# Performance work log

Hardware: AMD Instinct MI355X
Metric: run time of the kernel (lower is better)

The kernel has to match this reference:

```python
import jax, jax.numpy as jnp
from jax import lax
import numpy as np

UNITS, S, B, T = 64, 16, 512, 4096
LOG_2PI = float(np.log(2.0 * np.pi))


def setup_inputs() -> dict:
    key = jax.random.key(0)
    k1, k2 = jax.random.split(key)
    inputs = jax.random.normal(k1, (B, T), dtype=jnp.float32)
    # positive 'probs' (TFP Categorical takes log internally)
    hmm_params = jax.random.uniform(k2, (UNITS, S, S), dtype=jnp.float32,
                                    minval=1e-3, maxval=1.0)
    return {"inputs": inputs, "hmm_params": hmm_params}


def reference(inputs, hmm_params):
    # --- HMM parameters, as TFP builds them ---
    trans = hmm_params[0]                      # (S, S) unnormalized probs
    log_A = jnp.log(trans) - jnp.log(trans.sum(-1, keepdims=True))  # (S,S) row-normalized
    init = hmm_params[0, 0]                    # (S,)
    log_pi = jnp.log(init) - jnp.log(init.sum())
    # Emission: Normal(loc=0, scale=1) per state -> same logp for every state
    emit = -0.5 * inputs * inputs - 0.5 * LOG_2PI   # [B, T]
    emit = emit[:, :, None]                          # [B, T, 1] broadcasts over S

    # --- Viterbi forward (max-product) ---
    delta0 = log_pi[None, :] + emit[:, 0]            # [B, S]
    emit_seq = jnp.moveaxis(emit[:, 1:], 1, 0)       # [T-1, B, 1]

    def step(delta, e_t):
        scores = delta[:, :, None] + log_A[None, :, :]   # [B, S_prev, S_cur]
        psi = jnp.argmax(scores, axis=1).astype(jnp.int32)  # [B, S]
        delta_new = jnp.max(scores, axis=1) + e_t            # [B, S]
        return delta_new, psi

    deltaT, psis = lax.scan(step, delta0, emit_seq)  # psis: [T-1, B, S]

    # --- Backtrace ---
    zT = jnp.argmax(deltaT, axis=-1).astype(jnp.int32)   # [B]

    def back(z, psi):
        z_prev = jnp.take_along_axis(psi, z[:, None], axis=1)[:, 0]
        return z_prev, z_prev

    _, zs = lax.scan(back, zT, psis, reverse=True)   # zs: [T-1, B] = states t=0..T-2
    path = jnp.concatenate([zs.T, zT[:, None]], axis=1)  # [B, T]
    return path
```

## Files before the change

### kernel.cpp

```cpp
#include <hip/hip_runtime.h>
#include <math.h>

#define T_LEN 4096
#define B_SZ  512
#define CH    128
#define NCH   32
#define PITCH 129
#define PHASES 34

typedef unsigned uv2 __attribute__((ext_vector_type(2)));

__device__ __forceinline__ float emis(float xv) {
    float a = __fmul_rn(-0.5f, xv);
    float b = __fmul_rn(a, xv);
    return __fsub_rn(b, (float)0.9189385332046727);
}

#define DPP_ROR0(K, SRC) __builtin_amdgcn_update_dpp(0, (SRC), 0x120 + (K), 0xF, 0xF, false)
#define M3(x, y, z) fmaxf(fmaxf(x, y), z)

#define ADP(DST, K)                                                                   \
    asm("v_add_f32_dpp %0, %1, %2 row_ror:" #K " row_mask:0xf bank_mask:0xf"          \
        : "=v"(DST) : "v"(dr), "v"(a[K]))

#define STEPC(ET)                                                                     \
    {                                                                                 \
        float s0 = __fadd_rn(dr, a[0]);                                               \
        float s1, s2, s3, s4, s5, s6, s7;                                             \
        ADP(s1, 1); ADP(s2, 2); ADP(s3, 3); ADP(s4, 4);                               \
        ADP(s5, 5); ADP(s6, 6); ADP(s7, 7);                                           \
        float u0 = M3(s0, s1, s2), u1 = M3(s3, s4, s5), u2 = fmaxf(s6, s7);           \
        float own = M3(u0, u1, u2);                                                   \
        unsigned ou = __float_as_uint(own);                                           \
        uv2 rr = __builtin_amdgcn_permlane32_swap(ou, ou, false, false);              \
        float m = M3(__uint_as_float(rr[0]), __uint_as_float(rr[1]), own);            \
        float t8 = __int_as_float(__builtin_amdgcn_update_dpp(                        \
            0, __float_as_int(m), 0x128, 0xF, 0xF, false));                           \
        dr = __fadd_rn(hi32 ? t8 : m, ET);                                            \
    }

#define GRP4(QV, SLOTDW)                                                              \
    {                                                                                 \
        float4 dq;                                                                    \
        STEPC(QV.x) dq.x = dr; STEPC(QV.y) dq.y = dr;                                 \
        STEPC(QV.z) dq.z = dr; STEPC(QV.w) dq.w = dr;                                 \
        if (lo32) *(float4*)(db + (SLOTDW)) = dq;                                     \
    }

#define PERMSEL(V, Q)                                                                 \
    {                                                                                 \
        int sel_ = (V) & 7;                                                           \
        int lo_, hi_;                                                                 \
        asm("v_perm_b32 %0, %1, %2, %3" : "=v"(lo_) : "v"((Q).y), "v"((Q).x), "v"(sel_)); \
        asm("v_perm_b32 %0, %1, %2, %3" : "=v"(hi_) : "v"((Q).w), "v"((Q).z), "v"(sel_)); \
        V = (((V) & 8) ? hi_ : lo_) & 0xff;                                           \
    }

#define WALKN(BASE, CUR, PRE, POST, START)                                            \
    {                                                                                 \
        uint4 m_[8];                                                                  \
        _Pragma("unroll") for (int z_ = 0; z_ < 8; ++z_)                              \
            m_[z_] = *(const uint4*)((BASE) + ((START) - z_) * 16);                   \
        for (int r_ = (START); r_ >= 15; r_ -= 8) {                                   \
            uint4 n_[8];                                                              \
            _Pragma("unroll") for (int z_ = 0; z_ < 8; ++z_)                          \
                n_[z_] = *(const uint4*)((BASE) + (r_ - 8 - z_) * 16);                \
            _Pragma("unroll") for (int z_ = 0; z_ < 8; ++z_) {                        \
                PRE(r_ - z_, CUR) PERMSEL(CUR, m_[z_]) POST(r_ - z_, CUR)             \
            }                                                                         \
            _Pragma("unroll") for (int z_ = 0; z_ < 8; ++z_) m_[z_] = n_[z_];         \
        }                                                                             \
        _Pragma("unroll") for (int z_ = 0; z_ < 8; ++z_) {                            \
            PRE(7 - z_, CUR) PERMSEL(CUR, m_[z_]) POST(7 - z_, CUR)                   \
        }                                                                             \
    }

#define NIBHOP(V, Q) (V) = (int)(((Q) >> ((unsigned)(V) << 2)) & 15ull);

#define NWALKN(BASE, CUR, POST, START)                                                \
    {                                                                                 \
        const unsigned long long* bb_ = (BASE);                                       \
        unsigned long long m_[8];                                                     \
        _Pragma("unroll") for (int z_ = 0; z_ < 8; ++z_) m_[z_] = bb_[(START) - z_];  \
        for (int r_ = (START); r_ >= 15; r_ -= 8) {                                   \
            unsigned long long n_[8];                                                 \
            _Pragma("unroll") for (int z_ = 0; z_ < 8; ++z_) n_[z_] = bb_[r_ - 8 - z_]; \
            _Pragma("unroll") for (int z_ = 0; z_ < 8; ++z_) {                        \
                NIBHOP(CUR, m_[z_]) POST(r_ - z_, CUR)                                \
            }                                                                         \
            _Pragma("unroll") for (int z_ = 0; z_ < 8; ++z_) m_[z_] = n_[z_];         \
        }                                                                             \
        _Pragma("unroll") for (int z_ = 0; z_ < 8; ++z_) {                            \
            NIBHOP(CUR, m_[z_]) POST(7 - z_, CUR)                                     \
        }                                                                             \
    }

#define NOPX(r, c)
#define EBL_PRE(r, c) eb[r] = (unsigned char)(c);
#define OUT_POST(r, c) ob[r] = (c);

#define RLF(V, L) __int_as_float(__builtin_amdgcn_readlane(__float_as_int(V), (L)))

#define PSI2_I(I, V, BL)                                                              \
    {                                                                                 \
        float cs_ = RLF(V, (BL) + (I));                                               \
        float sA_ = __fadd_rn(ddA[I], cs_);                                           \
        if (sA_ > bestA) argA = I;                           \
        bestA = fmaxf(bestA, sA_);                                                    \
        float sB_ = __fadd_rn(ddB[I], cs_);                                           \
        if (sB_ > bestB) argB = I;                                                    \
        bestB = fmaxf(bestB, sB_);                                                    \
    }

#define PSI2_J(JJ, V)                                                                 \
    {                                                                                 \
        float c0_ = RLF(V, (((JJ) & 3) * 16) + 0);                                    \
        float bestA = __fadd_rn(ddA[0], c0_); int argA = 0;                           \
        float bestB = __fadd_rn(ddB[0], c0_); int argB = 0;                           \
        PSI2_I(1, V, ((JJ) & 3) * 16)  PSI2_I(2, V, ((JJ) & 3) * 16)                  \
        PSI2_I(3, V, ((JJ) & 3) * 16)  PSI2_I(4, V, ((JJ) & 3) * 16)                  \
        PSI2_I(5, V, ((JJ) & 3) * 16)  PSI2_I(6, V, ((JJ) & 3) * 16)                  \
        PSI2_I(7, V, ((JJ) & 3) * 16)  PSI2_I(8, V, ((JJ) & 3) * 16)                  \
        PSI2_I(9, V, ((JJ) & 3) * 16)  PSI2_I(10, V, ((JJ) & 3) * 16)                 \
        PSI2_I(11, V, ((JJ) & 3) * 16) PSI2_I(12, V, ((JJ) & 3) * 16)                 \
        PSI2_I(13, V, ((JJ) & 3) * 16) PSI2_I(14, V, ((JJ) & 3) * 16)                 \
        PSI2_I(15, V, ((JJ) & 3) * 16)                                                \
        pkA |= (unsigned long long)argA << ((JJ) * 4);                                \
        pkB |= (unsigned long long)argB << ((JJ) * 4);                                \
    }

__global__ __launch_bounds__(256) void k_fused(const float* __restrict__ x,
                                               const float* __restrict__ hmm,
                                               int* __restrict__ out) {
    __shared__ __align__(16) float dbuf[2][2][16][132];
    __shared__ unsigned long long pnib[2][NCH * PITCH];
    __shared__ uint4 Mlv[2][NCH];
    __shared__ unsigned char Ebl[2][NCH];
    __shared__ float carry_l[2][16];
    __shared__ float logA_l[256];
    __shared__ float logAT_l[256];
    __shared__ __align__(16) float Ebuf[4][2][CH];

    const int tid = threadIdx.x;
    const int wave = tid >> 6;
    const int blk = blockIdx.x;

    {
        const int pi = tid >> 4, pj = tid & 15;
        const float* row = hmm + pi * 16;
        float r8[8];
#pragma unroll
        for (int k = 0; k < 8; ++k) r8[k] = __fadd_rn(row[k], row[k + 8]);
        float s = __fadd_rn(
            __fadd_rn(__fadd_rn(r8[0], r8[1]), __fadd_rn(r8[2], r8[3])),
            __fadd_rn(__fadd_rn(r8[4], r8[5]), __fadd_rn(r8[6], r8[7])));
        float la = (float)log((double)row[pj]);
        float ls = (float)log((double)s);
        float v = __fsub_rn(la, ls);
        logA_l[tid] = v;
        logAT_l[pj * 16 + pi] = v;
        const int cc0 = tid >> 7, gp = (tid >> 6) & 1, l0 = tid & 63;
        const size_t xb = (size_t)(blk * 2 + gp) * T_LEN + CH * cc0 + l0 + 1;
        Ebuf[cc0][gp][l0]      = emis(x[xb]);
        Ebuf[cc0][gp][l0 + 64] = emis(x[xb + 64]);
    }
    __syncthreads();

    if (wave == 0) {
        asm volatile("s_setprio 3");
        const int j = tid & 15;
        const int g = (tid >> 4) & 1;
        const int h = tid >> 5;
        const bool lo32 = (tid < 32);
        const bool hi32 = (tid >= 32);
        const int jh = (j + 8 * h) & 15;
        float a[8];
        float dr;
        float4 q0, q1, q2, q3;
        {
            a[0] = logA_l[jh * 16 + j];
#define LOADA(K) { int sk = DPP_ROR0(K, jh); a[K] = logA_l[sk * 16 + j]; }
            LOADA(1) LOADA(2) LOADA(3) LOADA(4) LOADA(5) LOADA(6) LOADA(7)
#undef LOADA
            const int b = blk * 2 + g;
            float e0 = emis(x[(size_t)b * T_LEN]);
            dr = __fadd_rn(logA_l[jh], e0);
            const float4* e0p = (const float4*)&Ebuf[0][g][0];
            q0 = e0p[0]; q1 = e0p[1]; q2 = e0p[2]; q3 = e0p[3];
        }
        for (int p = 0; p < PHASES; ++p) {
            __syncthreads();
            if (p < NCH) {
                float* db = &dbuf[p & 1][g][j][0];
                if (lo32) db[128] = dr;
                const float4* ecur = (const float4*)&Ebuf[p & 3][g][0];
                const float4* enxt = (const float4*)&Ebuf[(p + 1) & 3][g][0];
                if (p < NCH - 1) {
#pragma clang loop unroll(disable)
                    for (int ii = 0; ii < 7; ++ii) {
                        GRP4(q0, ii * 16 + 0)  q0 = ecur[(ii + 1) * 4 + 0];
                        GRP4(q1, ii * 16 + 4)  q1 = ecur[(ii + 1) * 4 + 1];
                        GRP4(q2, ii * 16 + 8)  q2 = ecur[(ii + 1) * 4 + 2];
                        GRP4(q3, ii * 16 + 12) q3 = ecur[(ii + 1) * 4 + 3];
                    }
                    GRP4(q0, 112) q0 = enxt[0];
                    GRP4(q1, 116) q1 = enxt[1];
                    GRP4(q2, 120) q2 = enxt[2];
                    GRP4(q3, 124) q3 = enxt[3];
                } else {
#pragma clang loop unroll(disable)
                    for (int ii = 0; ii < 7; ++ii) {
                        GRP4(q0, ii * 16 + 0)  q0 = ecur[(ii + 1) * 4 + 0];
                        GRP4(q1, ii * 16 + 4)  q1 = ecur[(ii + 1) * 4 + 1];
                        GRP4(q2, ii * 16 + 8)  q2 = ecur[(ii + 1) * 4 + 2];
                        GRP4(q3, ii * 16 + 12) q3 = ecur[(ii + 1) * 4 + 3];
                    }
                    GRP4(q0, 112) GRP4(q1, 116) GRP4(q2, 120)
                    STEPC(q3.x) if (lo32) db[124] = dr;
                    STEPC(q3.y) if (lo32) db[125] = dr;
                    STEPC(q3.z) if (lo32) db[126] = dr;
                }
            }
        }
        if (lo32) carry_l[g][j] = dr;
    } else if (wave <= 2) {
        const int g2 = wave - 1;
        const int r = tid & 63;
        float vq0 = logAT_l[r];
        float vq1 = logAT_l[64 + r];
        float vq2 = logAT_l[128 + r];
        float vq3 = logAT_l[192 + r];
        for (int p = 0; p < PHASES; ++p) {
            __syncthreads();
            const int c = p - 1;
            if (c >= 0 && c < NCH) {
                const int q = c & 1;
                const int rsA = (r == 0) ? 128 : (r - 1);
                const int rsB = r + 63;
                float ddA[16], ddB[16];
#pragma unroll
                for (int i = 0; i < 16; ++i) {
                    ddA[i] = dbuf[q][g2][i][rsA];
                    ddB[i] = dbuf[q][g2][i][rsB];
                }
                asm volatile("" : "+v"(vq0), "+v"(vq1), "+v"(vq2), "+v"(vq3));
                unsigned long long pkA = 0ull, pkB = 0ull;
                PSI2_J(0, vq0)  PSI2_J(1, vq0)  PSI2_J(2, vq0)  PSI2_J(3, vq0)
                PSI2_J(4, vq1)  PSI2_J(5, vq1)  PSI2_J(6, vq1)  PSI2_J(7, vq1)
                PSI2_J(8, vq2)  PSI2_J(9, vq2)  PSI2_J(10, vq2) PSI2_J(11, vq2)
                PSI2_J(12, vq3) PSI2_J(13, vq3) PSI2_J(14, vq3) PSI2_J(15, vq3)
                if (c == NCH - 1 && r == 63) pkB = 0xFEDCBA9876543210ull;
                pnib[g2][c * PITCH + r]      = pkA;
                pnib[g2][c * PITCH + r + 64] = pkB;
            }
        }
    } else {
        const int l = tid - 192;
        const int g3 = l >> 4, z = l & 15;
        for (int p = 0; p < PHASES; ++p) {
            __syncthreads();
            const int cc = p + 2;
            if (cc < NCH) {
                const int t1 = CH * cc + l + 1;
                const int t2 = t1 + 64;
                Ebuf[cc & 3][0][l] = emis(x[(size_t)(blk * 2 + 0) * T_LEN + t1]);
                Ebuf[cc & 3][1][l] = emis(x[(size_t)(blk * 2 + 1) * T_LEN + t1]);
                if (t2 <= T_LEN - 1) {
                    Ebuf[cc & 3][0][l + 64] = emis(x[(size_t)(blk * 2 + 0) * T_LEN + t2]);
                    Ebuf[cc & 3][1][l + 64] = emis(x[(size_t)(blk * 2 + 1) * T_LEN + t2]);
                }
            }
            const int c = p - 2;
            if (c >= 0 && l < 32) {
                int cur = z;
                NWALKN(&pnib[g3][c * PITCH], cur, NOPX, 127)
                ((unsigned char*)&Mlv[g3][c])[z] = (unsigned char)cur;
            }
        }
    }

    __syncthreads();
    if (tid < 2) {
        const int g = tid;
        float best = carry_l[g][0]; int zT = 0;
#pragma unroll
        for (int i = 1; i < 16; ++i) {
            float s = carry_l[g][i];
            if (s > best) zT = i;
            best = fmaxf(best, s);
        }
        int z = zT;
        unsigned char* eb = &Ebl[g][0];
        WALKN((const unsigned char*)&Mlv[g][0], z, EBL_PRE, NOPX, NCH - 1)
    }
    __syncthreads();
    if (tid < 64) {
        const int g = tid >> 5, c = tid & 31;
        int* ob = out + (size_t)(blk * 2 + g) * T_LEN + c * CH;
        int cur = Ebl[g][c];
        NWALKN(&pnib[g][c * PITCH], cur, OUT_POST, 127)
    }
}

extern "C" void kernel_launch(void* const* d_in, const int* in_sizes, int n_in,
                              void* d_out, int out_size, void* d_ws, size_t ws_size,
                              hipStream_t stream) {
    (void)in_sizes; (void)n_in; (void)out_size; (void)d_ws; (void)ws_size;
    const float* x   = (const float*)d_in[0];
    const float* hmm = (const float*)d_in[1];
    int* out = (int*)d_out;

    hipLaunchKernelGGL(k_fused, dim3(B_SZ / 2), dim3(256), 0, stream, x, hmm, out);
}
```

Baseline: 302.0 us.

## Process one batch row per block instead of two, doubling grid size

Each block now handles a single sequence rather than two, so the grid covers all 512 rows with 512 blocks. The forward wave uses only 16 lanes per step, the psi waves each take half of the 128 time positions for that one row, and all shared-memory buffers shrink by half. This cuts the serial work per block and spreads the rows over more blocks, trading for lower lane utilisation in the DPP recurrence wave and for doubling the per-block setup and sync overhead.

```diff
diff --git a/kernel.cpp b/kernel.cpp
--- a/kernel.cpp
+++ b/kernel.cpp
@@ -44,7 +44,7 @@
         float4 dq;                                                                    \
         STEPC(QV.x) dq.x = dr; STEPC(QV.y) dq.y = dr;                                 \
         STEPC(QV.z) dq.z = dr; STEPC(QV.w) dq.w = dr;                                 \
-        if (lo32) *(float4*)(db + (SLOTDW)) = dq;                                     \
+        if (lo16) *(float4*)(db + (SLOTDW)) = dq;                                     \
     }
 
 #define PERMSEL(V, Q)                                                                 \
@@ -101,49 +101,44 @@
 
 #define RLF(V, L) __int_as_float(__builtin_amdgcn_readlane(__float_as_int(V), (L)))
 
-#define PSI2_I(I, V, BL)                                                              \
-    {                                                                                 \
-        float cs_ = RLF(V, (BL) + (I));                                               \
-        float sA_ = __fadd_rn(ddA[I], cs_);                                           \
-        if (sA_ > bestA) argA = I;                           \
-        bestA = fmaxf(bestA, sA_);                                                    \
-        float sB_ = __fadd_rn(ddB[I], cs_);                                           \
-        if (sB_ > bestB) argB = I;                                                    \
-        bestB = fmaxf(bestB, sB_);                                                    \
-    }
-
-#define PSI2_J(JJ, V)                                                                 \
-    {                                                                                 \
-        float c0_ = RLF(V, (((JJ) & 3) * 16) + 0);                                    \
-        float bestA = __fadd_rn(ddA[0], c0_); int argA = 0;                           \
-        float bestB = __fadd_rn(ddB[0], c0_); int argB = 0;                           \
-        PSI2_I(1, V, ((JJ) & 3) * 16)  PSI2_I(2, V, ((JJ) & 3) * 16)                  \
-        PSI2_I(3, V, ((JJ) & 3) * 16)  PSI2_I(4, V, ((JJ) & 3) * 16)                  \
-        PSI2_I(5, V, ((JJ) & 3) * 16)  PSI2_I(6, V, ((JJ) & 3) * 16)                  \
-        PSI2_I(7, V, ((JJ) & 3) * 16)  PSI2_I(8, V, ((JJ) & 3) * 16)                  \
-        PSI2_I(9, V, ((JJ) & 3) * 16)  PSI2_I(10, V, ((JJ) & 3) * 16)                 \
-        PSI2_I(11, V, ((JJ) & 3) * 16) PSI2_I(12, V, ((JJ) & 3) * 16)                 \
-        PSI2_I(13, V, ((JJ) & 3) * 16) PSI2_I(14, V, ((JJ) & 3) * 16)                 \
-        PSI2_I(15, V, ((JJ) & 3) * 16)                                                \
-        pkA |= (unsigned long long)argA << ((JJ) * 4);                                \
-        pkB |= (unsigned long long)argB << ((JJ) * 4);                                \
+#define PSI1_I(I, V, BL)                                                              \
+    {                                                                                 \
+        float s_ = __fadd_rn(dd[I], RLF(V, (BL) + (I)));                              \
+        if (s_ > best) arg = I;                              \
+        best = fmaxf(best, s_);                                                       \
+    }
+
+#define PSI1_J(JJ, V)                                                                 \
+    {                                                                                 \
+        float best = __fadd_rn(dd[0], RLF(V, (((JJ) & 3) * 16) + 0));                 \
+        int arg = 0;                                                                  \
+        PSI1_I(1, V, ((JJ) & 3) * 16)  PSI1_I(2, V, ((JJ) & 3) * 16)                  \
+        PSI1_I(3, V, ((JJ) & 3) * 16)  PSI1_I(4, V, ((JJ) & 3) * 16)                  \
+        PSI1_I(5, V, ((JJ) & 3) * 16)  PSI1_I(6, V, ((JJ) & 3) * 16)                  \
+        PSI1_I(7, V, ((JJ) & 3) * 16)  PSI1_I(8, V, ((JJ) & 3) * 16)                  \
+        PSI1_I(9, V, ((JJ) & 3) * 16)  PSI1_I(10, V, ((JJ) & 3) * 16)                 \
+        PSI1_I(11, V, ((JJ) & 3) * 16) PSI1_I(12, V, ((JJ) & 3) * 16)                 \
+        PSI1_I(13, V, ((JJ) & 3) * 16) PSI1_I(14, V, ((JJ) & 3) * 16)                 \
+        PSI1_I(15, V, ((JJ) & 3) * 16)                                                \
+        pk |= (unsigned long long)arg << ((JJ) * 4);                                  \
     }
 
 __global__ __launch_bounds__(256) void k_fused(const float* __restrict__ x,
                                                const float* __restrict__ hmm,
                                                int* __restrict__ out) {
-    __shared__ __align__(16) float dbuf[2][2][16][132];
-    __shared__ unsigned long long pnib[2][NCH * PITCH];
-    __shared__ uint4 Mlv[2][NCH];
-    __shared__ unsigned char Ebl[2][NCH];
-    __shared__ float carry_l[2][16];
+    __shared__ __align__(16) float dbuf[2][16][132];
+    __shared__ unsigned long long pnib[NCH * PITCH];
+    __shared__ uint4 Mlv[NCH];
+    __shared__ unsigned char Ebl[NCH];
+    __shared__ float carry_l[16];
     __shared__ float logA_l[256];
     __shared__ float logAT_l[256];
-    __shared__ __align__(16) float Ebuf[4][2][CH];
+    __shared__ __align__(16) float Ebuf[4][CH];
 
     const int tid = threadIdx.x;
     const int wave = tid >> 6;
     const int blk = blockIdx.x;
+    const size_t xb = (size_t)blk * T_LEN;
 
     {
         const int pi = tid >> 4, pj = tid & 15;
@@ -159,19 +154,16 @@
         float v = __fsub_rn(la, ls);
         logA_l[tid] = v;
         logAT_l[pj * 16 + pi] = v;
-        const int cc0 = tid >> 7, gp = (tid >> 6) & 1, l0 = tid & 63;
-        const size_t xb = (size_t)(blk * 2 + gp) * T_LEN + CH * cc0 + l0 + 1;
-        Ebuf[cc0][gp][l0]      = emis(x[xb]);
-        Ebuf[cc0][gp][l0 + 64] = emis(x[xb + 64]);
+        const int cc0 = tid >> 7, pos = tid & 127;
+        Ebuf[cc0][pos] = emis(x[xb + CH * cc0 + pos + 1]);
     }
     __syncthreads();
 
     if (wave == 0) {
         asm volatile("s_setprio 3");
         const int j = tid & 15;
-        const int g = (tid >> 4) & 1;
         const int h = tid >> 5;
-        const bool lo32 = (tid < 32);
+        const bool lo16 = (tid < 16);
         const bool hi32 = (tid >= 32);
         const int jh = (j + 8 * h) & 15;
         float a[8];
@@ -182,19 +174,18 @@
 #define LOADA(K) { int sk = DPP_ROR0(K, jh); a[K] = logA_l[sk * 16 + j]; }
             LOADA(1) LOADA(2) LOADA(3) LOADA(4) LOADA(5) LOADA(6) LOADA(7)
 #undef LOADA
-            const int b = blk * 2 + g;
-            float e0 = emis(x[(size_t)b * T_LEN]);
+            float e0 = emis(x[xb]);
             dr = __fadd_rn(logA_l[jh], e0);
-            const float4* e0p = (const float4*)&Ebuf[0][g][0];
+            const float4* e0p = (const float4*)&Ebuf[0][0];
             q0 = e0p[0]; q1 = e0p[1]; q2 = e0p[2]; q3 = e0p[3];
         }
         for (int p = 0; p < PHASES; ++p) {
             __syncthreads();
             if (p < NCH) {
-                float* db = &dbuf[p & 1][g][j][0];
-                if (lo32) db[128] = dr;
-                const float4* ecur = (const float4*)&Ebuf[p & 3][g][0];
-                const float4* enxt = (const float4*)&Ebuf[(p + 1) & 3][g][0];
+                float* db = &dbuf[p & 1][j][0];
+                if (lo16) db[128] = dr;
+                const float4* ecur = (const float4*)&Ebuf[p & 3][0];
+                const float4* enxt = (const float4*)&Ebuf[(p + 1) & 3][0];
                 if (p < NCH - 1) {
 #pragma clang loop unroll(disable)
                     for (int ii = 0; ii < 7; ++ii) {
@@ -216,15 +207,15 @@
                         GRP4(q3, ii * 16 + 12) q3 = ecur[(ii + 1) * 4 + 3];
                     }
                     GRP4(q0, 112) GRP4(q1, 116) GRP4(q2, 120)
-                    STEPC(q3.x) if (lo32) db[124] = dr;
-                    STEPC(q3.y) if (lo32) db[125] = dr;
-                    STEPC(q3.z) if (lo32) db[126] = dr;
+                    STEPC(q3.x) if (lo16) db[124] = dr;
+                    STEPC(q3.y) if (lo16) db[125] = dr;
+                    STEPC(q3.z) if (lo16) db[126] = dr;
                 }
             }
         }
-        if (lo32) carry_l[g][j] = dr;
+        if (lo16) carry_l[j] = dr;
     } else if (wave <= 2) {
-        const int g2 = wave - 1;
+        const int half = wave - 1;
         const int r = tid & 63;
         float vq0 = logAT_l[r];
         float vq1 = logAT_l[64 + r];
@@ -235,70 +226,59 @@
             const int c = p - 1;
             if (c >= 0 && c < NCH) {
                 const int q = c & 1;
-                const int rsA = (r == 0) ? 128 : (r - 1);
-                const int rsB = r + 63;
-                float ddA[16], ddB[16];
+                const int rs = half ? (r + 63) : ((r == 0) ? 128 : (r - 1));
+                float dd[16];
 #pragma unroll
-                for (int i = 0; i < 16; ++i) {
-                    ddA[i] = dbuf[q][g2][i][rsA];
-                    ddB[i] = dbuf[q][g2][i][rsB];
-                }
+                for (int i = 0; i < 16; ++i) dd[i] = dbuf[q][i][rs];
                 asm volatile("" : "+v"(vq0), "+v"(vq1), "+v"(vq2), "+v"(vq3));
-                unsigned long long pkA = 0ull, pkB = 0ull;
-                PSI2_J(0, vq0)  PSI2_J(1, vq0)  PSI2_J(2, vq0)  PSI2_J(3, vq0)
-                PSI2_J(4, vq1)  PSI2_J(5, vq1)  PSI2_J(6, vq1)  PSI2_J(7, vq1)
-                PSI2_J(8, vq2)  PSI2_J(9, vq2)  PSI2_J(10, vq2) PSI2_J(11, vq2)
-                PSI2_J(12, vq3) PSI2_J(13, vq3) PSI2_J(14, vq3) PSI2_J(15, vq3)
-                if (c == NCH - 1 && r == 63) pkB = 0xFEDCBA9876543210ull;
-                pnib[g2][c * PITCH + r]      = pkA;
-                pnib[g2][c * PITCH + r + 64] = pkB;
+                unsigned long long pk = 0ull;
+                PSI1_J(0, vq0)  PSI1_J(1, vq0)  PSI1_J(2, vq0)  PSI1_J(3, vq0)
+                PSI1_J(4, vq1)  PSI1_J(5, vq1)  PSI1_J(6, vq1)  PSI1_J(7, vq1)
+                PSI1_J(8, vq2)  PSI1_J(9, vq2)  PSI1_J(10, vq2) PSI1_J(11, vq2)
+                PSI1_J(12, vq3) PSI1_J(13, vq3) PSI1_J(14, vq3) PSI1_J(15, vq3)
+                if (half && c == NCH - 1 && r == 63) pk = 0xFEDCBA9876543210ull;
+                pnib[c * PITCH + half * 64 + r] = pk;
             }
         }
     } else {
-        const int l = tid - 192;
-        const int g3 = l >> 4, z = l & 15;
+        const int l = tid & 63;
         for (int p = 0; p < PHASES; ++p) {
             __syncthreads();
             const int cc = p + 2;
             if (cc < NCH) {
                 const int t1 = CH * cc + l + 1;
                 const int t2 = t1 + 64;
-                Ebuf[cc & 3][0][l] = emis(x[(size_t)(blk * 2 + 0) * T_LEN + t1]);
-                Ebuf[cc & 3][1][l] = emis(x[(size_t)(blk * 2 + 1) * T_LEN + t1]);
-                if (t2 <= T_LEN - 1) {
-                    Ebuf[cc & 3][0][l + 64] = emis(x[(size_t)(blk * 2 + 0) * T_LEN + t2]);
-                    Ebuf[cc & 3][1][l + 64] = emis(x[(size_t)(blk * 2 + 1) * T_LEN + t2]);
-                }
+                Ebuf[cc & 3][l] = emis(x[xb + t1]);
+                if (t2 <= T_LEN - 1) Ebuf[cc & 3][l + 64] = emis(x[xb + t2]);
             }
             const int c = p - 2;
-            if (c >= 0 && l < 32) {
-                int cur = z;
-                NWALKN(&pnib[g3][c * PITCH], cur, NOPX, 127)
-                ((unsigned char*)&Mlv[g3][c])[z] = (unsigned char)cur;
+            if (c >= 0 && l < 16) {
+                int cur = l;
+                NWALKN(&pnib[c * PITCH], cur, NOPX, 127)
+                ((unsigned char*)&Mlv[c])[l] = (unsigned char)cur;
             }
         }
     }
 
     __syncthreads();
-    if (tid < 2) {
-        const int g = tid;
-        float best = carry_l[g][0]; int zT = 0;
+    if (tid == 0) {
+        float best = carry_l[0]; int zT = 0;
 #pragma unroll
         for (int i = 1; i < 16; ++i) {
-            float s = carry_l[g][i];
+            float s = carry_l[i];
             if (s > best) zT = i;
             best = fmaxf(best, s);
         }
         int z = zT;
-        unsigned char* eb = &Ebl[g][0];
-        WALKN((const unsigned char*)&Mlv[g][0], z, EBL_PRE, NOPX, NCH - 1)
+        unsigned char* eb = &Ebl[0];
+        WALKN((const unsigned char*)&Mlv[0], z, EBL_PRE, NOPX, NCH - 1)
     }
     __syncthreads();
-    if (tid < 64) {
-        const int g = tid >> 5, c = tid & 31;
-        int* ob = out + (size_t)(blk * 2 + g) * T_LEN + c * CH;
-        int cur = Ebl[g][c];
-        NWALKN(&pnib[g][c * PITCH], cur, OUT_POST, 127)
+    if (tid < NCH) {
+        const int c = tid;
+        int* ob = out + xb + c * CH;
+        int cur = Ebl[c];
+        NWALKN(&pnib[c * PITCH], cur, OUT_POST, 127)
     }
 }
 
@@ -310,5 +290,5 @@
     const float* hmm = (const float*)d_in[1];
     int* out = (int*)d_out;
 
-    hipLaunchKernelGGL(k_fused, dim3(B_SZ / 2), dim3(256), 0, stream, x, hmm, out);
+    hipLaunchKernelGGL(k_fused, dim3(B_SZ), dim3(256), 0, stream, x, hmm, out);
 }
```

Measured after the change: 295.5 us. 2.1% less time.

## Alternate two lane layouts per Viterbi step to drop the final DPP select

Applied to the files above, without the earlier changes.

The serial max-plus recurrence now alternates between two lane-to-state mappings (A and B), each with its own preloaded transition table. Odd steps no longer need the trailing row-rotate and the hi/lo lane select after the cross-half max. Even steps instead do a rotate before the permlane32 swap plus a compare-select to choose the cross value. The goal is to shorten the critical dependency chain of each step. It doubles the register tables, and the equality-based select could pick the wrong value when the two swapped values tie.

```diff
diff --git a/kernel.cpp b/kernel.cpp
--- a/kernel.cpp
+++ b/kernel.cpp
@@ -19,31 +19,45 @@
 #define DPP_ROR0(K, SRC) __builtin_amdgcn_update_dpp(0, (SRC), 0x120 + (K), 0xF, 0xF, false)
 #define M3(x, y, z) fmaxf(fmaxf(x, y), z)
 
-#define ADP(DST, K)                                                                   \
+#define ADPX(DST, K, TBL)                                                             \
     asm("v_add_f32_dpp %0, %1, %2 row_ror:" #K " row_mask:0xf bank_mask:0xf"          \
-        : "=v"(DST) : "v"(dr), "v"(a[K]))
-
-#define STEPC(ET)                                                                     \
-    {                                                                                 \
-        float s0 = __fadd_rn(dr, a[0]);                                               \
+        : "=v"(DST) : "v"(dr), "v"(TBL[K]))
+
+#define OWN8(TBL)                                                                     \
+        float s0 = __fadd_rn(dr, TBL[0]);                                             \
         float s1, s2, s3, s4, s5, s6, s7;                                             \
-        ADP(s1, 1); ADP(s2, 2); ADP(s3, 3); ADP(s4, 4);                               \
-        ADP(s5, 5); ADP(s6, 6); ADP(s7, 7);                                           \
+        ADPX(s1, 1, TBL); ADPX(s2, 2, TBL); ADPX(s3, 3, TBL); ADPX(s4, 4, TBL);       \
+        ADPX(s5, 5, TBL); ADPX(s6, 6, TBL); ADPX(s7, 7, TBL);                         \
         float u0 = M3(s0, s1, s2), u1 = M3(s3, s4, s5), u2 = fmaxf(s6, s7);           \
-        float own = M3(u0, u1, u2);                                                   \
-        unsigned ou = __float_as_uint(own);                                           \
-        uv2 rr = __builtin_amdgcn_permlane32_swap(ou, ou, false, false);              \
+        float own = M3(u0, u1, u2);
+
+#define STEPC_A(ET)                                                                   \
+    {                                                                                 \
+        OWN8(aA)                                                                      \
+        float rot = __int_as_float(__builtin_amdgcn_update_dpp(                       \
+            0, __float_as_int(own), 0x128, 0xF, 0xF, false));                         \
+        unsigned rb = __float_as_uint(rot);                                           \
+        uv2 rr = __builtin_amdgcn_permlane32_swap(rb, rb, false, false);              \
+        float r0 = __uint_as_float(rr[0]), r1 = __uint_as_float(rr[1]);               \
+        float cross = (r0 == rot) ? r1 : r0;       \
+        float m = fmaxf(own, cross);                                                  \
+        dr = __fadd_rn(m, ET);                                                        \
+    }
+
+#define STEPC_B(ET)                                                                   \
+    {                                                                                 \
+        OWN8(aB)                                                                      \
+        unsigned ob = __float_as_uint(own);                                           \
+        uv2 rr = __builtin_amdgcn_permlane32_swap(ob, ob, false, false);              \
         float m = M3(__uint_as_float(rr[0]), __uint_as_float(rr[1]), own);            \
-        float t8 = __int_as_float(__builtin_amdgcn_update_dpp(                        \
-            0, __float_as_int(m), 0x128, 0xF, 0xF, false));                           \
-        dr = __fadd_rn(hi32 ? t8 : m, ET);                                            \
+        dr = __fadd_rn(m, ET);                                                        \
     }
 
 #define GRP4(QV, SLOTDW)                                                              \
     {                                                                                 \
         float4 dq;                                                                    \
-        STEPC(QV.x) dq.x = dr; STEPC(QV.y) dq.y = dr;                                 \
-        STEPC(QV.z) dq.z = dr; STEPC(QV.w) dq.w = dr;                                 \
+        STEPC_A(QV.x) dq.x = dr; STEPC_B(QV.y) dq.y = dr;                             \
+        STEPC_A(QV.z) dq.z = dr; STEPC_B(QV.w) dq.w = dr;                             \
         if (lo32) *(float4*)(db + (SLOTDW)) = dq;                                     \
     }
 
@@ -172,19 +186,20 @@
         const int g = (tid >> 4) & 1;
         const int h = tid >> 5;
         const bool lo32 = (tid < 32);
-        const bool hi32 = (tid >= 32);
         const int jh = (j + 8 * h) & 15;
-        float a[8];
+        float aA[8], aB[8];
         float dr;
         float4 q0, q1, q2, q3;
         {
-            a[0] = logA_l[jh * 16 + j];
-#define LOADA(K) { int sk = DPP_ROR0(K, jh); a[K] = logA_l[sk * 16 + j]; }
-            LOADA(1) LOADA(2) LOADA(3) LOADA(4) LOADA(5) LOADA(6) LOADA(7)
-#undef LOADA
+            aA[0] = logA_l[j * 16 + jh];
+            aB[0] = logA_l[jh * 16 + j];
+#define LOADT(K) { int sA_ = DPP_ROR0(K, j);  aA[K] = logA_l[sA_ * 16 + jh];          \
+                   int sB_ = DPP_ROR0(K, jh); aB[K] = logA_l[sB_ * 16 + j]; }
+            LOADT(1) LOADT(2) LOADT(3) LOADT(4) LOADT(5) LOADT(6) LOADT(7)
+#undef LOADT
             const int b = blk * 2 + g;
             float e0 = emis(x[(size_t)b * T_LEN]);
-            dr = __fadd_rn(logA_l[jh], e0);
+            dr = __fadd_rn(logA_l[j], e0);
             const float4* e0p = (const float4*)&Ebuf[0][g][0];
             q0 = e0p[0]; q1 = e0p[1]; q2 = e0p[2]; q3 = e0p[3];
         }
@@ -216,9 +231,9 @@
                         GRP4(q3, ii * 16 + 12) q3 = ecur[(ii + 1) * 4 + 3];
                     }
                     GRP4(q0, 112) GRP4(q1, 116) GRP4(q2, 120)
-                    STEPC(q3.x) if (lo32) db[124] = dr;
-                    STEPC(q3.y) if (lo32) db[125] = dr;
-                    STEPC(q3.z) if (lo32) db[126] = dr;
+                    STEPC_A(q3.x) if (lo32) db[124] = dr;
+                    STEPC_B(q3.y) if (lo32) db[125] = dr;
+                    STEPC_A(q3.z) if (lo32) db[126] = dr;
                 }
             }
         }
```

After: 296.0 us. 2.0% less time.
